# Performance work log

Hardware: AMD Instinct MI355X
Metric: run time of the kernel (lower is better)

The kernel has to match this reference:

```python
import jax, jax.numpy as jnp
import numpy as np


def setup_inputs() -> dict:
    key = jax.random.key(0)
    ks = jax.random.split(key, 7)
    B, S, H, T = 128, 512, 768, 3
    return {
        "inputs": jax.random.normal(ks[0], (B, S, H), dtype=jnp.float32),
        "y": jax.random.randint(ks[1], (B, S), 0, T, dtype=jnp.int64),
        "W": jax.random.normal(ks[2], (T, H), dtype=jnp.float32) * 0.02,
        "b": jax.random.normal(ks[3], (T,), dtype=jnp.float32) * 0.02,
        "transitions": jax.random.normal(ks[4], (T, T), dtype=jnp.float32),
        "start_transitions": jax.random.normal(ks[5], (T,), dtype=jnp.float32),
        "stop_transitions": jax.random.normal(ks[6], (T,), dtype=jnp.float32),
    }


def _crf_loss(feats, tags, transitions, start_transitions, stop_transitions):
    # feats: (B, S, T) emissions; tags: (B, S) int labels
    B, S, T = feats.shape
    # ---- gold sequence score ----
    emit = jnp.take_along_axis(feats, tags[:, :, None], axis=2)[..., 0]  # (B, S)
    trans = transitions[tags[:, :-1], tags[:, 1:]]                        # (B, S-1)
    seq_score = (emit.sum(-1) + trans.sum(-1)
                 + start_transitions[tags[:, 0]]
                 + stop_transitions[tags[:, -1]])                          # (B,)
    # ---- log partition via forward algorithm (scan over time) ----
    a0 = feats[:, 0] + start_transitions[None, :]  # (B, T)

    def step(a, feat_t):
        # a: (B, T) alpha at t-1; feat_t: (B, T) emissions at t
        # scores[b, i, j] = a[b, i] + transitions[i, j] + feat_t[b, j]
        a_new = jax.nn.logsumexp(a[:, :, None] + transitions[None, :, :]
                                 + feat_t[:, None, :], axis=1)
        return a_new, None

    aT, _ = jax.lax.scan(step, a0, jnp.swapaxes(feats[:, 1:], 0, 1))
    log_z = jax.nn.logsumexp(aT + stop_transitions[None, :], axis=1)  # (B,)
    return -(seq_score - log_z).mean()


def reference(inputs, y, W, b, transitions, start_transitions, stop_transitions):
    # Linear projection: (B, S, H) @ (H, T) + (T,)
    prediction = jnp.einsum("bsh,th->bst", inputs, W) + b
    crf_loss = _crf_loss(prediction, y, transitions, start_transitions,
                         stop_transitions)
    return (prediction, crf_loss)
```

## Files before the change

### kernel.cpp

```cpp
#include <hip/hip_runtime.h>

constexpr int NB = 128;
constexpr int NS = 512;
constexpr int NH = 768;
constexpr int NT = 3;
constexpr int ROWS = NB * NS;
constexpr int NCH = 64;
constexpr int CHL = 8;
constexpr float NEG = -1e30f;

__device__ __forceinline__ float lse3(float x0, float x1, float x2) {
    float m = fmaxf(x0, fmaxf(x1, x2));
    return m + __logf(__expf(x0 - m) + __expf(x1 - m) + __expf(x2 - m));
}

__device__ __forceinline__ float dot4(float4 a, float4 b) {
    return a.x * b.x + a.y * b.y + a.z * b.z + a.w * b.w;
}

__global__ __launch_bounds__(256) void pred_kernel(
    const float* __restrict__ x, const float* __restrict__ W,
    const float* __restrict__ bias, float* __restrict__ out)
{
    const int lane   = threadIdx.x & 63;
    const int nwaves = gridDim.x * 4;
    const int gw     = blockIdx.x * 4 + (threadIdx.x >> 6);

    const float4* W4 = (const float4*)W;
    float4 w[3][3];
#pragma unroll
    for (int t = 0; t < 3; ++t)
#pragma unroll
        for (int c = 0; c < 3; ++c)
            w[t][c] = W4[t * 192 + c * 64 + lane];
    const float b0 = bias[0], b1 = bias[1], b2 = bias[2];

    const float4* X4 = (const float4*)x;
    int row = gw;
    if (row >= ROWS) return;
    int base = row * 192 + lane;
    float4 v0 = X4[base], v1 = X4[base + 64], v2 = X4[base + 128];

    while (true) {
        const int nrow = row + nwaves;
        const bool more = nrow < ROWS;
        float4 t0, t1, t2;
        if (more) {
            const int nb = nrow * 192 + lane;
            t0 = X4[nb]; t1 = X4[nb + 64]; t2 = X4[nb + 128];
        }
        float acc0 = dot4(v0, w[0][0]) + dot4(v1, w[0][1]) + dot4(v2, w[0][2]);
        float acc1 = dot4(v0, w[1][0]) + dot4(v1, w[1][1]) + dot4(v2, w[1][2]);
        float acc2 = dot4(v0, w[2][0]) + dot4(v1, w[2][1]) + dot4(v2, w[2][2]);
#pragma unroll
        for (int off = 32; off >= 1; off >>= 1) {
            acc0 += __shfl_xor(acc0, off, 64);
            acc1 += __shfl_xor(acc1, off, 64);
            acc2 += __shfl_xor(acc2, off, 64);
        }
        if (lane < 3) {
            float a = (lane == 0) ? acc0 + b0 : ((lane == 1) ? acc1 + b1 : acc2 + b2);
            out[(size_t)row * 3 + lane] = a;
        }
        if (!more) break;
        v0 = t0; v1 = t1; v2 = t2; row = nrow;
    }
}

__global__ __launch_bounds__(256) void crf_scan_kernel(
    const float* __restrict__ feats, const int* __restrict__ y,
    const float* __restrict__ trans, float* __restrict__ ws_m,
    float* __restrict__ ws_p)
{
    __shared__ float sTr[9];
    if (threadIdx.x < 9) sTr[threadIdx.x] = trans[threadIdx.x];
    __syncthreads();

    const int gtid = blockIdx.x * 256 + threadIdx.x;
    const int e  = gtid % 3;
    const int bc = gtid / 3;
    const int b  = bc >> 6;
    const int c  = bc & 63;

    const float T00 = sTr[0], T01 = sTr[1], T02 = sTr[2];
    const float T10 = sTr[3], T11 = sTr[4], T12 = sTr[5];
    const float T20 = sTr[6], T21 = sTr[7], T22 = sTr[8];

    const float* fb = feats + (size_t)b * NS * NT;
    const int*   yb = y + b * NS;

    float a0 = (e == 0) ? 0.f : NEG;
    float a1 = (e == 1) ? 0.f : NEG;
    float a2 = (e == 2) ? 0.f : NEG;

    const int s_begin = (c == 0) ? 1 : c * CHL;
    const int s_end   = c * CHL + CHL;

    float sc = 0.f;
    int prev = yb[s_begin - 1];
    if (c == 0) {
        float g0 = fb[0], g1 = fb[1], g2 = fb[2];
        sc = (prev == 0) ? g0 : ((prev == 1) ? g1 : g2);
    }

    for (int s = s_begin; s < s_end; ++s) {
        const float f0 = fb[s * 3], f1 = fb[s * 3 + 1], f2 = fb[s * 3 + 2];
        const int tg = yb[s];
        sc += ((tg == 0) ? f0 : ((tg == 1) ? f1 : f2)) + sTr[prev * 3 + tg];
        prev = tg;
        const float n0 = f0 + lse3(a0 + T00, a1 + T10, a2 + T20);
        const float n1 = f1 + lse3(a0 + T01, a1 + T11, a2 + T21);
        const float n2 = f2 + lse3(a0 + T02, a1 + T12, a2 + T22);
        a0 = n0; a1 = n1; a2 = n2;
    }

    float4* dst = (float4*)(ws_m + (size_t)(b * NCH + c) * 12) + e;
    *dst = make_float4(a0, a1, a2, 0.f);
    if (e == 0) ws_p[b * NCH + c] = sc;
}

__global__ __launch_bounds__(128) void crf_combine_kernel(
    const float* __restrict__ feats, const int* __restrict__ y,
    const float* __restrict__ ws_m, const float* __restrict__ ws_p,
    const float* __restrict__ startt, const float* __restrict__ stopt,
    float* __restrict__ loss_out)
{
    __shared__ float partial[2];
    const int b = threadIdx.x;

    const float st0 = startt[0], st1 = startt[1], st2 = startt[2];
    const float sp0 = stopt[0],  sp1 = stopt[1],  sp2 = stopt[2];

    const float* fb = feats + (size_t)b * NS * NT;
    float a0 = fb[0] + st0, a1 = fb[1] + st1, a2 = fb[2] + st2;

    const float4* M = (const float4*)(ws_m + (size_t)b * NCH * 12);
    const float*  P = ws_p + b * NCH;

    float4 m0 = M[0], m1 = M[1], m2 = M[2];
    float  pp = P[0];
    float  sc = 0.f;

#pragma unroll 4
    for (int c = 0; c < NCH; ++c) {
        float4 u0, u1, u2; float up;
        if (c < NCH - 1) {
            u0 = M[(c + 1) * 3]; u1 = M[(c + 1) * 3 + 1]; u2 = M[(c + 1) * 3 + 2];
            up = P[c + 1];
        }
        sc += pp;
        const float n0 = lse3(a0 + m0.x, a1 + m1.x, a2 + m2.x);
        const float n1 = lse3(a0 + m0.y, a1 + m1.y, a2 + m2.y);
        const float n2 = lse3(a0 + m0.z, a1 + m1.z, a2 + m2.z);
        a0 = n0; a1 = n1; a2 = n2;
        m0 = u0; m1 = u1; m2 = u2; pp = up;
    }

    const float logz = lse3(a0 + sp0, a1 + sp1, a2 + sp2);
    const int y0 = y[b * NS], yl = y[b * NS + NS - 1];
    const float seq = sc + ((y0 == 0) ? st0 : ((y0 == 1) ? st1 : st2))
                         + ((yl == 0) ? sp0 : ((yl == 1) ? sp1 : sp2));
    float val = seq - logz;

#pragma unroll
    for (int off = 32; off >= 1; off >>= 1)
        val += __shfl_xor(val, off, 64);
    if ((threadIdx.x & 63) == 0) partial[threadIdx.x >> 6] = val;
    __syncthreads();
    if (threadIdx.x == 0)
        loss_out[0] = -(partial[0] + partial[1]) / (float)NB;
}

extern "C" void kernel_launch(void* const* d_in, const int* in_sizes, int n_in,
                              void* d_out, int out_size, void* d_ws, size_t ws_size,
                              hipStream_t stream)
{
    const float* x      = (const float*)d_in[0];
    const int*   y      = (const int*)d_in[1];
    const float* W      = (const float*)d_in[2];
    const float* bias   = (const float*)d_in[3];
    const float* trans  = (const float*)d_in[4];
    const float* startt = (const float*)d_in[5];
    const float* stopt  = (const float*)d_in[6];

    float* out      = (float*)d_out;
    float* loss_out = out + (size_t)NB * NS * NT;

    float* ws_m = (float*)d_ws;
    float* ws_p = ws_m + (size_t)NB * NCH * 12;

    pred_kernel<<<1024, 256, 0, stream>>>(x, W, bias, out);
    crf_scan_kernel<<<(NB * NCH * 3) / 256, 256, 0, stream>>>(out, y, trans, ws_m, ws_p);
    crf_combine_kernel<<<1, 128, 0, stream>>>(out, y, ws_m, ws_p, startt, stopt, loss_out);
}
```

Measured before the change: 321.8 us.

## Process two rows per wave in projection and vectorize CRF chunk loads

```diff
diff --git a/kernel.cpp b/kernel.cpp
--- a/kernel.cpp
+++ b/kernel.cpp
@@ -18,13 +18,18 @@
     return a.x * b.x + a.y * b.y + a.z * b.z + a.w * b.w;
 }
 
+__device__ __forceinline__ float sel3(int t, float a, float b, float c) {
+    return (t == 0) ? a : ((t == 1) ? b : c);
+}
+
 __global__ __launch_bounds__(256) void pred_kernel(
     const float* __restrict__ x, const float* __restrict__ W,
     const float* __restrict__ bias, float* __restrict__ out)
 {
-    const int lane   = threadIdx.x & 63;
-    const int nwaves = gridDim.x * 4;
-    const int gw     = blockIdx.x * 4 + (threadIdx.x >> 6);
+    const int lane = threadIdx.x & 63;
+    const int gw   = blockIdx.x * 4 + (threadIdx.x >> 6);
+    const int nw   = gridDim.x * 4;
+    const int stride = nw * 2;
 
     const float4* W4 = (const float4*)W;
     float4 w[3][3];
@@ -36,34 +41,49 @@
     const float b0 = bias[0], b1 = bias[1], b2 = bias[2];
 
     const float4* X4 = (const float4*)x;
-    int row = gw;
+    int row = gw * 2;
     if (row >= ROWS) return;
-    int base = row * 192 + lane;
-    float4 v0 = X4[base], v1 = X4[base + 64], v2 = X4[base + 128];
+
+    float4 vA[3], vB[3];
+    {
+        const int ba = row * 192 + lane;
+#pragma unroll
+        for (int c = 0; c < 3; ++c) { vA[c] = X4[ba + c * 64]; vB[c] = X4[ba + 192 + c * 64]; }
+    }
 
     while (true) {
-        const int nrow = row + nwaves;
+        const int nrow = row + stride;
         const bool more = nrow < ROWS;
-        float4 t0, t1, t2;
+        float4 tA[3], tB[3];
         if (more) {
             const int nb = nrow * 192 + lane;
-            t0 = X4[nb]; t1 = X4[nb + 64]; t2 = X4[nb + 128];
-        }
-        float acc0 = dot4(v0, w[0][0]) + dot4(v1, w[0][1]) + dot4(v2, w[0][2]);
-        float acc1 = dot4(v0, w[1][0]) + dot4(v1, w[1][1]) + dot4(v2, w[1][2]);
-        float acc2 = dot4(v0, w[2][0]) + dot4(v1, w[2][1]) + dot4(v2, w[2][2]);
+#pragma unroll
+            for (int c = 0; c < 3; ++c) { tA[c] = X4[nb + c * 64]; tB[c] = X4[nb + 192 + c * 64]; }
+        }
+        float a0 = dot4(vA[0], w[0][0]) + dot4(vA[1], w[0][1]) + dot4(vA[2], w[0][2]);
+        float a1 = dot4(vA[0], w[1][0]) + dot4(vA[1], w[1][1]) + dot4(vA[2], w[1][2]);
+        float a2 = dot4(vA[0], w[2][0]) + dot4(vA[1], w[2][1]) + dot4(vA[2], w[2][2]);
+        float c0 = dot4(vB[0], w[0][0]) + dot4(vB[1], w[0][1]) + dot4(vB[2], w[0][2]);
+        float c1 = dot4(vB[0], w[1][0]) + dot4(vB[1], w[1][1]) + dot4(vB[2], w[1][2]);
+        float c2 = dot4(vB[0], w[2][0]) + dot4(vB[1], w[2][1]) + dot4(vB[2], w[2][2]);
 #pragma unroll
         for (int off = 32; off >= 1; off >>= 1) {
-            acc0 += __shfl_xor(acc0, off, 64);
-            acc1 += __shfl_xor(acc1, off, 64);
-            acc2 += __shfl_xor(acc2, off, 64);
-        }
-        if (lane < 3) {
-            float a = (lane == 0) ? acc0 + b0 : ((lane == 1) ? acc1 + b1 : acc2 + b2);
-            out[(size_t)row * 3 + lane] = a;
+            a0 += __shfl_xor(a0, off, 64);
+            a1 += __shfl_xor(a1, off, 64);
+            a2 += __shfl_xor(a2, off, 64);
+            c0 += __shfl_xor(c0, off, 64);
+            c1 += __shfl_xor(c1, off, 64);
+            c2 += __shfl_xor(c2, off, 64);
+        }
+        if (lane < 6) {
+            float v = (lane == 0) ? a0 + b0 : (lane == 1) ? a1 + b1 : (lane == 2) ? a2 + b2
+                    : (lane == 3) ? c0 + b0 : (lane == 4) ? c1 + b1 : c2 + b2;
+            out[(size_t)row * 3 + lane] = v;
         }
         if (!more) break;
-        v0 = t0; v1 = t1; v2 = t2; row = nrow;
+#pragma unroll
+        for (int c = 0; c < 3; ++c) { vA[c] = tA[c]; vB[c] = tB[c]; }
+        row = nrow;
     }
 }
 
@@ -89,24 +109,40 @@
     const float* fb = feats + (size_t)b * NS * NT;
     const int*   yb = y + b * NS;
 
+    float ff[24];
+    {
+        float4* fv = (float4*)ff;
+        const float4* src = (const float4*)(fb + c * CHL * NT);
+#pragma unroll
+        for (int i = 0; i < 6; ++i) fv[i] = src[i];
+    }
+    int yy[8];
+    {
+        int4* yv = (int4*)yy;
+        const int4* ys = (const int4*)(yb + c * CHL);
+        yv[0] = ys[0]; yv[1] = ys[1];
+    }
+
     float a0 = (e == 0) ? 0.f : NEG;
     float a1 = (e == 1) ? 0.f : NEG;
     float a2 = (e == 2) ? 0.f : NEG;
 
-    const int s_begin = (c == 0) ? 1 : c * CHL;
-    const int s_end   = c * CHL + CHL;
-
     float sc = 0.f;
-    int prev = yb[s_begin - 1];
+    int prev;
     if (c == 0) {
-        float g0 = fb[0], g1 = fb[1], g2 = fb[2];
-        sc = (prev == 0) ? g0 : ((prev == 1) ? g1 : g2);
-    }
-
-    for (int s = s_begin; s < s_end; ++s) {
-        const float f0 = fb[s * 3], f1 = fb[s * 3 + 1], f2 = fb[s * 3 + 2];
-        const int tg = yb[s];
-        sc += ((tg == 0) ? f0 : ((tg == 1) ? f1 : f2)) + sTr[prev * 3 + tg];
+        prev = yy[0];
+        sc = sel3(prev, ff[0], ff[1], ff[2]);
+    } else {
+        prev = yb[c * CHL - 1];
+    }
+    const int sl0 = (c == 0) ? 1 : 0;
+
+#pragma unroll
+    for (int sl = 0; sl < CHL; ++sl) {
+        if (sl < sl0) continue;
+        const float f0 = ff[sl * 3], f1 = ff[sl * 3 + 1], f2 = ff[sl * 3 + 2];
+        const int tg = yy[sl];
+        sc += sel3(tg, f0, f1, f2) + sTr[prev * 3 + tg];
         prev = tg;
         const float n0 = f0 + lse3(a0 + T00, a1 + T10, a2 + T20);
         const float n1 = f1 + lse3(a0 + T01, a1 + T11, a2 + T21);
@@ -143,7 +179,7 @@
 
 #pragma unroll 4
     for (int c = 0; c < NCH; ++c) {
-        float4 u0, u1, u2; float up;
+        float4 u0 = m0, u1 = m1, u2 = m2; float up = pp;
         if (c < NCH - 1) {
             u0 = M[(c + 1) * 3]; u1 = M[(c + 1) * 3 + 1]; u2 = M[(c + 1) * 3 + 2];
             up = P[c + 1];
```

After: 321.5 us. About the same (-0.1%).
